# Kernel optimization log

Measured on AMD Instinct MI355X. Metric: run time of the kernel, lower is better.

The kernel has to match this reference:

```python
import jax, jax.numpy as jnp
import numpy as np

N = 50000          # nodes
E = 800000         # edges (avg degree 16)
F_IN = 64          # node feature dim
F_EDGE = 8         # edge feature dim (carried through, unused by EdgeConv)
DIMS = [64, 64, 64, 8]   # hidden layers + final num_classes layer (no BN)
EPS = 1e-5


def mish(x):
    return x * jnp.tanh(jax.nn.softplus(x))


def _init_layer(key, din, dout):
    k1, k2, k3, k4 = jax.random.split(key, 4)
    s1 = 1.0 / np.sqrt(2 * din)
    s2 = 1.0 / np.sqrt(dout)
    w1 = jax.random.uniform(k1, (2 * din, dout), jnp.float32, -s1, s1)
    b1 = jax.random.uniform(k2, (dout,), jnp.float32, -s1, s1)
    w2 = jax.random.uniform(k3, (dout, dout), jnp.float32, -s2, s2)
    b2 = jax.random.uniform(k4, (dout,), jnp.float32, -s2, s2)
    return w1, b1, w2, b2


def setup_inputs() -> dict:
    key = jax.random.key(0)
    ks = jax.random.split(key, 8)
    inp = {
        "x": jax.random.normal(ks[0], (N, F_IN), jnp.float32),
        "edge_index": jax.random.randint(ks[1], (2, E), 0, N, jnp.int32),
        "edge_attr": jax.random.normal(ks[2], (E, F_EDGE), jnp.float32),
    }
    din = F_IN
    for l, dout in enumerate(DIMS):
        w1, b1, w2, b2 = _init_layer(jax.random.fold_in(ks[3], l), din, dout)
        inp[f"w1_{l}"] = w1
        inp[f"b1_{l}"] = b1
        inp[f"w2_{l}"] = w2
        inp[f"b2_{l}"] = b2
        if l < len(DIMS) - 1:  # BN on all but final classifier layer
            inp[f"g_{l}"] = jnp.ones((dout,), jnp.float32)
            inp[f"be_{l}"] = jnp.zeros((dout,), jnp.float32)
        din = dout
    return inp


def _forward(x, edge_index, params):
    src = edge_index[0]
    dst = edge_index[1]
    for (w1, b1, w2, b2, g, be) in params:
        xi = x[dst]                       # [E, din] target feats
        xj = x[src]                       # [E, din] source feats
        m = jnp.concatenate([xi, xj - xi], axis=-1)   # [E, 2*din]
        h = mish(m @ w1 + b1) @ w2 + b2               # [E, dout]
        agg = jax.ops.segment_max(h, dst, num_segments=N)
        x = jnp.where(jnp.isfinite(agg), agg, 0.0)    # empty segments -> 0
        if g is not None:                 # BatchNorm1d, batch stats (train fwd)
            mu = x.mean(axis=0)
            var = x.var(axis=0)
            x = (x - mu) * jax.lax.rsqrt(var + EPS) * g + be
    return x


def reference(x, edge_index, edge_attr,
              w1_0, b1_0, w2_0, b2_0, g_0, be_0,
              w1_1, b1_1, w2_1, b2_1, g_1, be_1,
              w1_2, b1_2, w2_2, b2_2, g_2, be_2,
              w1_3, b1_3, w2_3, b2_3):
    params = [
        (w1_0, b1_0, w2_0, b2_0, g_0, be_0),
        (w1_1, b1_1, w2_1, b2_1, g_1, be_1),
        (w1_2, b1_2, w2_2, b2_2, g_2, be_2),
        (w1_3, b1_3, w2_3, b2_3, None, None),
    ]
    return _forward(x, edge_index, params)
```

## Files before the change

### kernel.cpp

```cpp
#include <hip/hip_runtime.h>
#include <hip/hip_bf16.h>
#include <math.h>

#define NN 50000
#define EE 800000
#define NT (EE / 16)
#define NTN (NN / 16)

#define NBLK64 1536
#define NW64 (NBLK64 * 4)
#define B64 (NT / NW64)
#define R64 (NT % NW64)

#define NBF 196
#define NWF (NBF * 4)

typedef short s8v __attribute__((ext_vector_type(8)));
typedef float f4v __attribute__((ext_vector_type(4)));

__device__ __forceinline__ short f2bf(float f) {
    unsigned u = __float_as_uint(f);
    u += 0x7fffu + ((u >> 16) & 1u);
    return (short)(u >> 16);
}

__device__ __forceinline__ unsigned enc(float f) {
    unsigned u = __float_as_uint(f);
    return (u & 0x80000000u) ? ~u : (u | 0x80000000u);
}
__device__ __forceinline__ float dec(unsigned k) {
    if (k == 0u) return 0.0f;
    unsigned u = (k & 0x80000000u) ? (k & 0x7fffffffu) : ~k;
    return __uint_as_float(u);
}

__device__ __forceinline__ float mish_fast(float v) {
    float t = __expf(v);
    float s = t * (t + 2.0f);
    float r = v * s * __builtin_amdgcn_rcpf(s + 2.0f);
    return (v > 15.0f) ? v : r;
}

#define MFMA16(a, b, c) __builtin_amdgcn_mfma_f32_16x16x32_bf16(a, b, c, 0, 0, 0)


#define NBS 196

__global__ __launch_bounds__(256) void scan_part(const int* __restrict__ cnt,
                                                 int* __restrict__ part) {
    int t = threadIdx.x, i = blockIdx.x * 256 + t;
    __shared__ int ps[256];
    ps[t] = (i < NN) ? cnt[i] : 0;
    __syncthreads();
    for (int off = 128; off > 0; off >>= 1) {
        if (t < off) ps[t] += ps[t + off];
        __syncthreads();
    }
    if (t == 0) part[blockIdx.x] = ps[0];
}

__global__ __launch_bounds__(256) void scan_top(int* __restrict__ part) {
    int t = threadIdx.x;
    int v = (t < NBS) ? part[t] : 0;
    __shared__ int ps[256];
    ps[t] = v;
    __syncthreads();
    for (int off = 1; off < 256; off <<= 1) {
        int u = (t >= off) ? ps[t - off] : 0;
        __syncthreads();
        ps[t] += u;
        __syncthreads();
    }
    if (t < NBS) part[t] = ps[t] - v;
}

__global__ __launch_bounds__(256) void scan_fin(const int* __restrict__ cnt,
                                                const int* __restrict__ part,
                                                int* __restrict__ row_off,
                                                int* __restrict__ cur) {
    int t = threadIdx.x, i = blockIdx.x * 256 + t;
    int v = (i < NN) ? cnt[i] : 0;
    __shared__ int ps[256];
    ps[t] = v;
    __syncthreads();
    for (int off = 1; off < 256; off <<= 1) {
        int u = (t >= off) ? ps[t - off] : 0;
        __syncthreads();
        ps[t] += u;
        __syncthreads();
    }
    int excl = ps[t] - v + part[blockIdx.x];
    if (i < NN) {
        row_off[i] = excl;
        cur[i] = excl;
        if (i == NN - 1) row_off[NN] = excl + v;
    }
}

__global__ __launch_bounds__(256) void scatter_k(const int* __restrict__ ei,
                                                 int* __restrict__ cur,
                                                 int* __restrict__ csr_src,
                                                 int* __restrict__ csr_dst) {
    int e = blockIdx.x * 256 + threadIdx.x;
    if (e < EE) {
        int d = ei[EE + e];
        int p = atomicAdd(&cur[d], 1);
        csr_src[p] = ei[e];
        csr_dst[p] = d;
    }
}


__global__ __launch_bounds__(256)
void cvt_a0(const float* __restrict__ x, const float* __restrict__ w1,
            const float* __restrict__ b1, const int* __restrict__ ei,
            unsigned short* __restrict__ xb, float* __restrict__ a0,
            unsigned* __restrict__ y, unsigned* __restrict__ y8,
            int* __restrict__ cnt) {
    const int tid = threadIdx.x;
    const int lane = tid & 63;
    const int wid = blockIdx.x * 4 + (tid >> 6);
    const int i = lane & 15, q = lane >> 4;
    s8v wf[4][2];
#pragma unroll
    for (int nb = 0; nb < 4; nb++)
#pragma unroll
        for (int kh = 0; kh < 2; kh++)
#pragma unroll
            for (int j = 0; j < 8; j++) {
                int k = kh * 32 + q * 8 + j, n = nb * 16 + i;
                wf[nb][kh][j] = f2bf(w1[k * 64 + n] - w1[(64 + k) * 64 + n]);
            }
    float bia[4];
#pragma unroll
    for (int nb = 0; nb < 4; nb++) bia[nb] = b1[nb * 16 + i];

    for (int t = wid; t < NTN; t += NWF) {
        const int row = t * 16 + i;
        const float* xr = x + (size_t)row * 64 + q * 8;
        f4v x0 = *(const f4v*)xr,        f1 = *(const f4v*)(xr + 4);
        f4v x2 = *(const f4v*)(xr + 32), x3 = *(const f4v*)(xr + 36);
        s8v af0, af1;
#pragma unroll
        for (int j = 0; j < 4; j++) {
            af0[j] = f2bf(x0[j]); af0[4 + j] = f2bf(f1[j]);
            af1[j] = f2bf(x2[j]); af1[4 + j] = f2bf(x3[j]);
        }
        unsigned short* xw = xb + (size_t)row * 64 + q * 8;
        *(s8v*)xw = af0;
        *(s8v*)(xw + 32) = af1;
        const int rowq = t * 16 + q * 4;
#pragma unroll
        for (int nb = 0; nb < 4; nb++) {
            f4v c = {0.f, 0.f, 0.f, 0.f};
            c = MFMA16(af0, wf[nb][0], c);
            c = MFMA16(af1, wf[nb][1], c);
#pragma unroll
            for (int r = 0; r < 4; r++)
                a0[(size_t)(rowq + r) * 64 + i * 4 + nb] = c[r] + bia[nb];
        }
    }
    const int gt = blockIdx.x * 256 + tid, gs = NBF * 256;
    const uint4 z4 = {0u, 0u, 0u, 0u};
    uint4* y4 = (uint4*)y;
    uint4* y84 = (uint4*)y8;
    for (int idx = gt; idx < NN * 16; idx += gs) y4[idx] = z4;
    for (int idx = gt; idx < NN * 2; idx += gs)  y84[idx] = z4;
    for (int e = gt; e < EE; e += gs) atomicAdd(&cnt[ei[EE + e]], 1);
}


__global__ __launch_bounds__(256)
void bn_a0_64(unsigned* __restrict__ yk, const float* __restrict__ st,
              const float* __restrict__ g, const float* __restrict__ be,
              const float* __restrict__ w1n, const float* __restrict__ b1n,
              unsigned short* __restrict__ xbout, float* __restrict__ a0out) {
    __shared__ float sa[64], sb[64];
    const int tid = threadIdx.x;
    if (tid < 64) {
        float mu  = st[tid] * (1.0f / NN);
        float var = st[64 + tid] * (1.0f / NN) - mu * mu;
        float sc  = rsqrtf(var + 1e-5f) * g[tid];
        sa[tid] = sc;
        sb[tid] = be[tid] - mu * sc;
    }
    __syncthreads();
    const int lane = tid & 63;
    const int wid = blockIdx.x * 4 + (tid >> 6);
    const int i = lane & 15, q = lane >> 4;

    s8v wf[4][2];
#pragma unroll
    for (int nb = 0; nb < 4; nb++)
#pragma unroll
        for (int kh = 0; kh < 2; kh++)
#pragma unroll
            for (int j = 0; j < 8; j++) {
                int k = kh * 32 + q * 8 + j, n = nb * 16 + i;
                wf[nb][kh][j] = f2bf(w1n[k * 64 + n] - w1n[(64 + k) * 64 + n]);
            }
    float bia[4];
#pragma unroll
    for (int nb = 0; nb < 4; nb++) bia[nb] = b1n[nb * 16 + i];

    f4v a00 = *(const f4v*)(sa + q * 8),      a01 = *(const f4v*)(sa + q * 8 + 4);
    f4v a10 = *(const f4v*)(sa + 32 + q * 8), a11 = *(const f4v*)(sa + 36 + q * 8);
    f4v b00 = *(const f4v*)(sb + q * 8),      b01 = *(const f4v*)(sb + q * 8 + 4);
    f4v b10 = *(const f4v*)(sb + 32 + q * 8), b11 = *(const f4v*)(sb + 36 + q * 8);

    const uint4 z4 = {0u, 0u, 0u, 0u};
    for (int t = wid; t < NTN; t += NWF) {
        const int row = t * 16 + i;
        unsigned* yr = yk + (size_t)row * 64 + q * 8;
        uint4 u0 = *(const uint4*)yr,        u1 = *(const uint4*)(yr + 4);
        uint4 u2 = *(const uint4*)(yr + 32), u3 = *(const uint4*)(yr + 36);
        s8v af0, af1;
        af0[0] = f2bf(dec(u0.x) * a00[0] + b00[0]);
        af0[1] = f2bf(dec(u0.y) * a00[1] + b00[1]);
        af0[2] = f2bf(dec(u0.z) * a00[2] + b00[2]);
        af0[3] = f2bf(dec(u0.w) * a00[3] + b00[3]);
        af0[4] = f2bf(dec(u1.x) * a01[0] + b01[0]);
        af0[5] = f2bf(dec(u1.y) * a01[1] + b01[1]);
        af0[6] = f2bf(dec(u1.z) * a01[2] + b01[2]);
        af0[7] = f2bf(dec(u1.w) * a01[3] + b01[3]);
        af1[0] = f2bf(dec(u2.x) * a10[0] + b10[0]);
        af1[1] = f2bf(dec(u2.y) * a10[1] + b10[1]);
        af1[2] = f2bf(dec(u2.z) * a10[2] + b10[2]);
        af1[3] = f2bf(dec(u2.w) * a10[3] + b10[3]);
        af1[4] = f2bf(dec(u3.x) * a11[0] + b11[0]);
        af1[5] = f2bf(dec(u3.y) * a11[1] + b11[1]);
        af1[6] = f2bf(dec(u3.z) * a11[2] + b11[2]);
        af1[7] = f2bf(dec(u3.w) * a11[3] + b11[3]);

        unsigned short* xw = xbout + (size_t)row * 64 + q * 8;
        *(s8v*)xw = af0;
        *(s8v*)(xw + 32) = af1;
        *(uint4*)yr = z4;        *(uint4*)(yr + 4) = z4;
        *(uint4*)(yr + 32) = z4; *(uint4*)(yr + 36) = z4;

        const int rowq = t * 16 + q * 4;
#pragma unroll
        for (int nb = 0; nb < 4; nb++) {
            f4v c = {0.f, 0.f, 0.f, 0.f};
            c = MFMA16(af0, wf[nb][0], c);
            c = MFMA16(af1, wf[nb][1], c);
#pragma unroll
            for (int r = 0; r < 4; r++)
                a0out[(size_t)(rowq + r) * 64 + i * 4 + nb] = c[r] + bia[nb];
        }
    }
}


__global__ __launch_bounds__(256)
void bn_a0_8(unsigned* __restrict__ yk, const float* __restrict__ st,
             const float* __restrict__ g, const float* __restrict__ be,
             const float* __restrict__ w1n, const float* __restrict__ b1n,
             unsigned short* __restrict__ xbout, float* __restrict__ a08) {
    __shared__ float sa[64], sb[64];
    const int tid = threadIdx.x;
    if (tid < 64) {
        float mu  = st[tid] * (1.0f / NN);
        float var = st[64 + tid] * (1.0f / NN) - mu * mu;
        float sc  = rsqrtf(var + 1e-5f) * g[tid];
        sa[tid] = sc;
        sb[tid] = be[tid] - mu * sc;
    }
    __syncthreads();
    const int lane = tid & 63;
    const int wid = blockIdx.x * 4 + (tid >> 6);
    const int i = lane & 15, q = lane >> 4;

    s8v wf[2];
#pragma unroll
    for (int kh = 0; kh < 2; kh++)
#pragma unroll
        for (int j = 0; j < 8; j++) {
            int k = kh * 32 + q * 8 + j;
            wf[kh][j] = (i < 8) ? f2bf(w1n[k * 8 + i] - w1n[(64 + k) * 8 + i]) : (short)0;
        }
    const float bia = (i < 8) ? b1n[i] : 0.0f;

    f4v a00 = *(const f4v*)(sa + q * 8),      a01 = *(const f4v*)(sa + q * 8 + 4);
    f4v a10 = *(const f4v*)(sa + 32 + q * 8), a11 = *(const f4v*)(sa + 36 + q * 8);
    f4v b00 = *(const f4v*)(sb + q * 8),      b01 = *(const f4v*)(sb + q * 8 + 4);
    f4v b10 = *(const f4v*)(sb + 32 + q * 8), b11 = *(const f4v*)(sb + 36 + q * 8);

    for (int t = wid; t < NTN; t += NWF) {
        const int row = t * 16 + i;
        const unsigned* yr = yk + (size_t)row * 64 + q * 8;
        uint4 u0 = *(const uint4*)yr,        u1 = *(const uint4*)(yr + 4);
        uint4 u2 = *(const uint4*)(yr + 32), u3 = *(const uint4*)(yr + 36);
        s8v af0, af1;
        af0[0] = f2bf(dec(u0.x) * a00[0] + b00[0]);
        af0[1] = f2bf(dec(u0.y) * a00[1] + b00[1]);
        af0[2] = f2bf(dec(u0.z) * a00[2] + b00[2]);
        af0[3] = f2bf(dec(u0.w) * a00[3] + b00[3]);
        af0[4] = f2bf(dec(u1.x) * a01[0] + b01[0]);
        af0[5] = f2bf(dec(u1.y) * a01[1] + b01[1]);
        af0[6] = f2bf(dec(u1.z) * a01[2] + b01[2]);
        af0[7] = f2bf(dec(u1.w) * a01[3] + b01[3]);
        af1[0] = f2bf(dec(u2.x) * a10[0] + b10[0]);
        af1[1] = f2bf(dec(u2.y) * a10[1] + b10[1]);
        af1[2] = f2bf(dec(u2.z) * a10[2] + b10[2]);
        af1[3] = f2bf(dec(u2.w) * a10[3] + b10[3]);
        af1[4] = f2bf(dec(u3.x) * a11[0] + b11[0]);
        af1[5] = f2bf(dec(u3.y) * a11[1] + b11[1]);
        af1[6] = f2bf(dec(u3.z) * a11[2] + b11[2]);
        af1[7] = f2bf(dec(u3.w) * a11[3] + b11[3]);

        unsigned short* xw = xbout + (size_t)row * 64 + q * 8;
        *(s8v*)xw = af0;
        *(s8v*)(xw + 32) = af1;

        f4v c = {0.f, 0.f, 0.f, 0.f};
        c = MFMA16(af0, wf[0], c);
        c = MFMA16(af1, wf[1], c);
        if (i < 8) {
            const int rowq = t * 16 + q * 4;
#pragma unroll
            for (int r = 0; r < 4; r++)
                a08[(size_t)(rowq + r) * 8 + i] = c[r] + bia;
        }
    }
}


__global__ __launch_bounds__(256)
void edge_mfma64(const unsigned short* __restrict__ xb, const float* __restrict__ a0,
                 const float* __restrict__ w1, const float* __restrict__ w2,
                 const float* __restrict__ b2,
                 const int* __restrict__ csr_src, const int* __restrict__ csr_dst,
                 unsigned* __restrict__ y) {
    __shared__ float uld[4][16 * 68];
    __shared__ int dseg[4][2][20];
    __shared__ short w2l[8 * 64 * 8];
    const int lane = threadIdx.x & 63;
    const int wv = threadIdx.x >> 6;
    const int wid = blockIdx.x * 4 + wv;
    const int i = lane & 15, q = lane >> 4;
    float* up = &uld[wv][0];

    s8v w1f[4][2];
#pragma unroll
    for (int nb = 0; nb < 4; nb++)
#pragma unroll
        for (int kh = 0; kh < 2; kh++)
#pragma unroll
            for (int j = 0; j < 8; j++) {
                int k = kh * 32 + q * 8 + j, n = nb * 16 + i;
                w1f[nb][kh][j] = f2bf(w1[(64 + k) * 64 + n]);
            }
    {
        const int nb = wv;
#pragma unroll
        for (int kh = 0; kh < 2; kh++) {
            s8v uu;
#pragma unroll
            for (int j = 0; j < 8; j++) {
                int k = kh * 32 + q * 8 + j;
                uu[j] = f2bf(w2[k * 64 + nb * 16 + i]);
            }
            *(s8v*)(w2l + ((nb * 2 + kh) * 64 + lane) * 8) = uu;
        }
    }
    __syncthreads();

    const float b2c = b2[lane];

    int t = wid * B64 + (wid < R64 ? wid : R64);
    const int tend = t + B64 + (wid < R64 ? 1 : 0);

    s8v af0_c, af1_c;
    {
        int s0 = csr_src[t * 16 + i];
        const unsigned short* xr = xb + (size_t)s0 * 64;
        af0_c = *(const s8v*)(xr + q * 8);
        af1_c = *(const s8v*)(xr + 32 + q * 8);
    }
    int src_n = (t + 1 < tend) ? csr_src[(t + 1) * 16 + i] : 0;
    if (lane < 17) {
        int e = t * 16 + lane;
        dseg[wv][t & 1][lane] = (e < EE) ? csr_dst[e] : -1;
    }
    asm volatile("s_waitcnt lgkmcnt(0)" ::: "memory");
    int dq_c[4];
#pragma unroll
    for (int r = 0; r < 4; r++) dq_c[r] = dseg[wv][t & 1][q * 4 + r];
    f4v a0r_c[4];
#pragma unroll
    for (int r = 0; r < 4; r++)
        a0r_c[r] = *(const f4v*)(a0 + (size_t)dq_c[r] * 64 + i * 4);

    float run = -INFINITY;

    for (; t < tend; t++) {
        const bool has_n = (t + 1) < tend;
        int* dsg = &dseg[wv][t & 1][0];
        int* dsg_n = &dseg[wv][(t + 1) & 1][0];

        if (has_n && lane < 17) {
            int e = (t + 1) * 16 + lane;
            dsg_n[lane] = (e < EE) ? csr_dst[e] : -1;
        }
        s8v af0_n = {0,0,0,0,0,0,0,0}, af1_n = {0,0,0,0,0,0,0,0};
        if (has_n) {
            const unsigned short* xr = xb + (size_t)src_n * 64;
            af0_n = *(const s8v*)(xr + q * 8);
            af1_n = *(const s8v*)(xr + 32 + q * 8);
        }
        int src_nn = (t + 2 < tend) ? csr_src[(t + 2) * 16 + i] : 0;

        f4v c0 = {0.f, 0.f, 0.f, 0.f}, c1 = c0, c2 = c0, c3 = c0;
        c0 = MFMA16(af0_c, w1f[0][0], c0); c0 = MFMA16(af1_c, w1f[0][1], c0);
        c1 = MFMA16(af0_c, w1f[1][0], c1); c1 = MFMA16(af1_c, w1f[1][1], c1);
        c2 = MFMA16(af0_c, w1f[2][0], c2); c2 = MFMA16(af1_c, w1f[2][1], c2);
        c3 = MFMA16(af0_c, w1f[3][0], c3); c3 = MFMA16(af1_c, w1f[3][1], c3);

        asm volatile("" ::: "memory");
#pragma unroll
        for (int r = 0; r < 4; r++) {
            const int ro = (q * 4 + r) * 68 + i;
            up[ro +  0] = mish_fast(c0[r] + a0r_c[r][0]);
            up[ro + 16] = mish_fast(c1[r] + a0r_c[r][1]);
            up[ro + 32] = mish_fast(c2[r] + a0r_c[r][2]);
            up[ro + 48] = mish_fast(c3[r] + a0r_c[r][3]);
        }
        asm volatile("s_waitcnt lgkmcnt(0)" ::: "memory");

        int dq_n[4];
        f4v a0r_n[4];
        if (has_n) {
#pragma unroll
            for (int r = 0; r < 4; r++) dq_n[r] = dsg_n[q * 4 + r];
#pragma unroll
            for (int r = 0; r < 4; r++)
                a0r_n[r] = *(const f4v*)(a0 + (size_t)dq_n[r] * 64 + i * 4);
        }

        s8v uf[2];
#pragma unroll
        for (int kh = 0; kh < 2; kh++) {
            const f4v* rp = (const f4v*)(up + i * 68 + kh * 32 + q * 8);
            f4v v0 = rp[0], v1 = rp[1];
            s8v uu;
            uu[0] = f2bf(v0[0]); uu[1] = f2bf(v0[1]);
            uu[2] = f2bf(v0[2]); uu[3] = f2bf(v0[3]);
            uu[4] = f2bf(v1[0]); uu[5] = f2bf(v1[1]);
            uu[6] = f2bf(v1[2]); uu[7] = f2bf(v1[3]);
            uf[kh] = uu;
        }
        asm volatile("" ::: "memory");

        f4v cc[4];
#pragma unroll
        for (int nb = 0; nb < 4; nb++) {
            s8v b0 = *(const s8v*)(w2l + ((nb * 2 + 0) * 64 + lane) * 8);
            s8v b1v = *(const s8v*)(w2l + ((nb * 2 + 1) * 64 + lane) * 8);
            f4v c = {0.f, 0.f, 0.f, 0.f};
            c = MFMA16(uf[0], b0, c);
            c = MFMA16(uf[1], b1v, c);
            cc[nb] = c;
        }

#pragma unroll
        for (int nb = 0; nb < 4; nb++)
#pragma unroll
            for (int r = 0; r < 4; r++)
                up[(q * 4 + r) * 68 + nb * 16 + i] = cc[nb][r];
        asm volatile("s_waitcnt lgkmcnt(0)" ::: "memory");

        float v[16];
#pragma unroll
        for (int row = 0; row < 16; row++) v[row] = up[row * 68 + lane];

        int dcur = __builtin_amdgcn_readfirstlane(dsg[0]);
#pragma unroll
        for (int row = 0; row < 16; row++) {
            run = fmaxf(run, v[row]);
            int dn = (row < 15)
                     ? __builtin_amdgcn_readfirstlane(dsg[row + 1])
                     : (has_n ? __builtin_amdgcn_readfirstlane(dsg[16]) : -1);
            if (dcur != dn) {
                atomicMax(&y[(size_t)dcur * 64 + lane], enc(run + b2c));
                run = -INFINITY;
            }
            dcur = dn;
        }
        asm volatile("s_waitcnt lgkmcnt(0)" ::: "memory");

        src_n = src_nn;
        af0_c = af0_n; af1_c = af1_n;
#pragma unroll
        for (int r = 0; r < 4; r++) { dq_c[r] = dq_n[r]; a0r_c[r] = a0r_n[r]; }
    }
}


__global__ __launch_bounds__(256)
void edge_mfma16(const unsigned short* __restrict__ xb, const float* __restrict__ a0,
                 const float* __restrict__ w1, const float* __restrict__ w2,
                 const float* __restrict__ b2,
                 const int* __restrict__ csr_src, const int* __restrict__ csr_dst,
                 unsigned* __restrict__ y8) {
    __shared__ float uld[4][16 * 20];
    __shared__ int dseg[4][2][20];
    const int lane = threadIdx.x & 63;
    const int wv = threadIdx.x >> 6;
    const int wid = blockIdx.x * 4 + wv;
    const int i = lane & 15, q = lane >> 4;
    float* up = &uld[wv][0];

    s8v w1f[2], w2f;
#pragma unroll
    for (int kh = 0; kh < 2; kh++)
#pragma unroll
        for (int j = 0; j < 8; j++) {
            int k = kh * 32 + q * 8 + j;
            w1f[kh][j] = (i < 8) ? f2bf(w1[(64 + k) * 8 + i]) : (short)0;
        }
#pragma unroll
    for (int j = 0; j < 8; j++)
        w2f[j] = (q == 0 && i < 8) ? f2bf(w2[j * 8 + i]) : (short)0;
    const float b2c = (lane < 8) ? b2[lane] : 0.0f;

    int t = wid * B64 + (wid < R64 ? wid : R64);
    const int tend = t + B64 + (wid < R64 ? 1 : 0);

    s8v af0_c, af1_c;
    {
        int s0 = csr_src[t * 16 + i];
        const unsigned short* xr = xb + (size_t)s0 * 64;
        af0_c = *(const s8v*)(xr + q * 8);
        af1_c = *(const s8v*)(xr + 32 + q * 8);
    }
    int src_n = (t + 1 < tend) ? csr_src[(t + 1) * 16 + i] : 0;
    if (lane < 17) {
        int e = t * 16 + lane;
        dseg[wv][t & 1][lane] = (e < EE) ? csr_dst[e] : -1;
    }
    asm volatile("s_waitcnt lgkmcnt(0)" ::: "memory");
    int dq_c[4];
#pragma unroll
    for (int r = 0; r < 4; r++) dq_c[r] = dseg[wv][t & 1][q * 4 + r];
    float av_c[4];
#pragma unroll
    for (int r = 0; r < 4; r++)
        av_c[r] = (i < 8) ? a0[(size_t)dq_c[r] * 8 + i] : 0.0f;

    float run = -INFINITY;

    for (; t < tend; t++) {
        const bool has_n = (t + 1) < tend;
        int* dsg = &dseg[wv][t & 1][0];
        int* dsg_n = &dseg[wv][(t + 1) & 1][0];

        if (has_n && lane < 17) {
            int e = (t + 1) * 16 + lane;
            dsg_n[lane] = (e < EE) ? csr_dst[e] : -1;
        }
        s8v af0_n = {0,0,0,0,0,0,0,0}, af1_n = {0,0,0,0,0,0,0,0};
        if (has_n) {
            const unsigned short* xr = xb + (size_t)src_n * 64;
            af0_n = *(const s8v*)(xr + q * 8);
            af1_n = *(const s8v*)(xr + 32 + q * 8);
        }
        int src_nn = (t + 2 < tend) ? csr_src[(t + 2) * 16 + i] : 0;

        f4v c = {0.f, 0.f, 0.f, 0.f};
        c = MFMA16(af0_c, w1f[0], c);
        c = MFMA16(af1_c, w1f[1], c);

        asm volatile("" ::: "memory");
#pragma unroll
        for (int r = 0; r < 4; r++)
            up[(q * 4 + r) * 20 + i] = mish_fast(c[r] + av_c[r]);
        asm volatile("s_waitcnt lgkmcnt(0)" ::: "memory");

        int dq_n[4];
        float av_n[4] = {0, 0, 0, 0};
        if (has_n) {
#pragma unroll
            for (int r = 0; r < 4; r++) dq_n[r] = dsg_n[q * 4 + r];
#pragma unroll
            for (int r = 0; r < 4; r++)
                av_n[r] = (i < 8) ? a0[(size_t)dq_n[r] * 8 + i] : 0.0f;
        }

        s8v uf = {0,0,0,0,0,0,0,0};
        if (q < 2) {
            const f4v* rp = (const f4v*)(up + i * 20 + q * 8);
            f4v v0 = rp[0], v1 = rp[1];
            uf[0] = f2bf(v0[0]); uf[1] = f2bf(v0[1]);
            uf[2] = f2bf(v0[2]); uf[3] = f2bf(v0[3]);
            uf[4] = f2bf(v1[0]); uf[5] = f2bf(v1[1]);
            uf[6] = f2bf(v1[2]); uf[7] = f2bf(v1[3]);
        }
        asm volatile("" ::: "memory");

        f4v cc = {0.f, 0.f, 0.f, 0.f};
        cc = MFMA16(uf, w2f, cc);

#pragma unroll
        for (int r = 0; r < 4; r++)
            up[(q * 4 + r) * 20 + i] = cc[r];
        asm volatile("s_waitcnt lgkmcnt(0)" ::: "memory");

        float v[16];
#pragma unroll
        for (int row = 0; row < 16; row++) v[row] = up[row * 20 + (lane & 7)];

        int dcur = dsg[0];
#pragma unroll
        for (int row = 0; row < 16; row++) {
            run = fmaxf(run, v[row]);
            int dn = (row < 15) ? dsg[row + 1] : (has_n ? dsg[16] : -1);
            if (dcur != dn) {
                if (lane < 8)
                    atomicMax(&y8[(size_t)dcur * 8 + lane], enc(run + b2c));
                run = -INFINITY;
            }
            dcur = dn;
        }
        asm volatile("s_waitcnt lgkmcnt(0)" ::: "memory");

        src_n = src_nn;
        af0_c = af0_n; af1_c = af1_n;
#pragma unroll
        for (int r = 0; r < 4; r++) av_c[r] = av_n[r];
    }
}


__global__ __launch_bounds__(256)
void bn_stats(const unsigned* __restrict__ yk, float* __restrict__ st) {
    const int tid = threadIdx.x;
    const int c4 = (tid & 15) * 4;
    const int grp = tid >> 4;
    float s0 = 0, s1 = 0, s2 = 0, s3 = 0;
    float q0 = 0, q1 = 0, q2 = 0, q3 = 0;
    for (int n = blockIdx.x * 16 + grp; n < NN; n += gridDim.x * 16) {
        uint4 u = *(const uint4*)(yk + (size_t)n * 64 + c4);
        float v0 = dec(u.x), v1 = dec(u.y), v2 = dec(u.z), v3 = dec(u.w);
        s0 += v0; s1 += v1; s2 += v2; s3 += v3;
        q0 = fmaf(v0, v0, q0); q1 = fmaf(v1, v1, q1);
        q2 = fmaf(v2, v2, q2); q3 = fmaf(v3, v3, q3);
    }
    __shared__ float ls[256][4], lq[256][4];
    ls[tid][0] = s0; ls[tid][1] = s1; ls[tid][2] = s2; ls[tid][3] = s3;
    lq[tid][0] = q0; lq[tid][1] = q1; lq[tid][2] = q2; lq[tid][3] = q3;
    __syncthreads();
    if (tid < 64) {
        const int cg = tid >> 2, ce = tid & 3;
        float ss = 0, qq = 0;
        for (int g = 0; g < 16; g++) {
            ss += ls[g * 16 + cg][ce];
            qq += lq[g * 16 + cg][ce];
        }
        atomicAdd(&st[cg * 4 + ce], ss);
        atomicAdd(&st[64 + cg * 4 + ce], qq);
    }
}

__global__ __launch_bounds__(256)
void decode_out(const unsigned* __restrict__ y8, float* __restrict__ out) {
    int idx = blockIdx.x * 256 + threadIdx.x;
    if (idx < NN * 8) out[idx] = dec(y8[idx]);
}


extern "C" void kernel_launch(void* const* d_in, const int* in_sizes, int n_in,
                              void* d_out, int out_size, void* d_ws, size_t ws_size,
                              hipStream_t stream) {
    const float* x0 = (const float*)d_in[0];
    const int*   ei = (const int*)d_in[1];
    const float* w1[4] = {(const float*)d_in[3],  (const float*)d_in[9],
                          (const float*)d_in[15], (const float*)d_in[21]};
    const float* b1[4] = {(const float*)d_in[4],  (const float*)d_in[10],
                          (const float*)d_in[16], (const float*)d_in[22]};
    const float* w2[4] = {(const float*)d_in[5],  (const float*)d_in[11],
                          (const float*)d_in[17], (const float*)d_in[23]};
    const float* b2[4] = {(const float*)d_in[6],  (const float*)d_in[12],
                          (const float*)d_in[18], (const float*)d_in[24]};
    const float* gg[3] = {(const float*)d_in[7],  (const float*)d_in[13],
                          (const float*)d_in[19]};
    const float* be[3] = {(const float*)d_in[8],  (const float*)d_in[14],
                          (const float*)d_in[20]};

    char* p = (char*)d_ws;
    auto alloc = [&](size_t bytes) -> char* {
        char* r = p;
        p += (bytes + 255) & ~(size_t)255;
        return r;
    };
    int*      cnt     = (int*)alloc((size_t)NN * 4);
    int*      part    = (int*)alloc((size_t)NBS * 4);
    int*      row_off = (int*)alloc((size_t)(NN + 1) * 4);
    int*      cur     = (int*)alloc((size_t)NN * 4);
    int*      csr_s   = (int*)alloc((size_t)EE * 4);
    int*      csr_d   = (int*)alloc((size_t)EE * 4);
    float*    st      = (float*)alloc(3 * 128 * 4);
    float*    a0      = (float*)alloc((size_t)NN * 64 * 4);
    unsigned* y       = (unsigned*)alloc((size_t)NN * 64 * 4);
    unsigned* y8      = (unsigned*)alloc((size_t)NN * 8 * 4);
    unsigned short* xb0 = (unsigned short*)alloc((size_t)NN * 64 * 2);
    unsigned short* xbA = (unsigned short*)alloc((size_t)NN * 64 * 2);
    unsigned short* xbB = xb0;

    hipMemsetAsync(cnt, 0, (size_t)NN * 4, stream);
    hipMemsetAsync(st, 0, 3 * 128 * 4, stream);

    cvt_a0<<<NBF, 256, 0, stream>>>(x0, w1[0], b1[0], ei, xb0, a0, y, y8, cnt);

    scan_part<<<NBS, 256, 0, stream>>>(cnt, part);
    scan_top<<<1, 256, 0, stream>>>(part);
    scan_fin<<<NBS, 256, 0, stream>>>(cnt, part, row_off, cur);
    scatter_k<<<(EE + 255) / 256, 256, 0, stream>>>(ei, cur, csr_s, csr_d);

    edge_mfma64<<<NBLK64, 256, 0, stream>>>(xb0, a0, w1[0], w2[0], b2[0],
                                            csr_s, csr_d, y);
    bn_stats<<<256, 256, 0, stream>>>(y, st);
    bn_a0_64<<<NBF, 256, 0, stream>>>(y, st, gg[0], be[0], w1[1], b1[1], xbA, a0);

    edge_mfma64<<<NBLK64, 256, 0, stream>>>(xbA, a0, w1[1], w2[1], b2[1],
                                            csr_s, csr_d, y);
    bn_stats<<<256, 256, 0, stream>>>(y, st + 128);
    bn_a0_64<<<NBF, 256, 0, stream>>>(y, st + 128, gg[1], be[1], w1[2], b1[2], xbB, a0);

    edge_mfma64<<<NBLK64, 256, 0, stream>>>(xbB, a0, w1[2], w2[2], b2[2],
                                            csr_s, csr_d, y);
    bn_stats<<<256, 256, 0, stream>>>(y, st + 256);
    bn_a0_8<<<NBF, 256, 0, stream>>>(y, st + 256, gg[2], be[2], w1[3], b1[3], xbA, a0);

    edge_mfma16<<<NBLK64, 256, 0, stream>>>(xbA, a0, w1[3], w2[3], b2[3],
                                            csr_s, csr_d, y8);
    decode_out<<<(NN * 8 + 255) / 256, 256, 0, stream>>>(y8, (float*)d_out);
}
```

Before: 512.7 us.

## Pre-reduce segment max in MFMA registers before LDS transpose in edge_mfma64

Replaces the per-tile LDS write of all 16x64 edge outputs and the sequential 16-row scan with a two-level reduction. Each lane first folds its 4 accumulator rows by destination, using wave-wide any-checks and atomics on segment breaks. Only the 4 partial maxima per column are then staged through LDS and scanned, carrying the running max across tiles with a final flush atomic. This cuts LDS traffic and scalar readfirstlane work. The cost is divergent atomics inside the register scan and reliance on lanes within a quad sharing each row's destination indices.

```diff
diff --git a/kernel.cpp b/kernel.cpp
--- a/kernel.cpp
+++ b/kernel.cpp
@@ -340,6 +340,7 @@
     const int wid = blockIdx.x * 4 + wv;
     const int i = lane & 15, q = lane >> 4;
     float* up = &uld[wv][0];
+    float* spw = up;
 
     s8v w1f[4][2];
 #pragma unroll
@@ -366,7 +367,9 @@
     }
     __syncthreads();
 
-    const float b2c = b2[lane];
+    const float b2s = b2[lane];
+    const float b2n0 = b2[i],      b2n1 = b2[16 + i];
+    const float b2n2 = b2[32 + i], b2n3 = b2[48 + i];
 
     int t = wid * B64 + (wid < R64 ? wid : R64);
     const int tend = t + B64 + (wid < R64 ? 1 : 0);
@@ -379,10 +382,7 @@
         af1_c = *(const s8v*)(xr + 32 + q * 8);
     }
     int src_n = (t + 1 < tend) ? csr_src[(t + 1) * 16 + i] : 0;
-    if (lane < 17) {
-        int e = t * 16 + lane;
-        dseg[wv][t & 1][lane] = (e < EE) ? csr_dst[e] : -1;
-    }
+    if (lane < 16) dseg[wv][t & 1][lane] = csr_dst[t * 16 + lane];
     asm volatile("s_waitcnt lgkmcnt(0)" ::: "memory");
     int dq_c[4];
 #pragma unroll
@@ -392,17 +392,16 @@
     for (int r = 0; r < 4; r++)
         a0r_c[r] = *(const f4v*)(a0 + (size_t)dq_c[r] * 64 + i * 4);
 
-    float run = -INFINITY;
+    float runC = -INFINITY;
+    int dcC = dseg[wv][t & 1][0];
 
     for (; t < tend; t++) {
         const bool has_n = (t + 1) < tend;
-        int* dsg = &dseg[wv][t & 1][0];
+        const int* dsg = &dseg[wv][t & 1][0];
         int* dsg_n = &dseg[wv][(t + 1) & 1][0];
 
-        if (has_n && lane < 17) {
-            int e = (t + 1) * 16 + lane;
-            dsg_n[lane] = (e < EE) ? csr_dst[e] : -1;
-        }
+        if (has_n && lane < 16) dsg_n[lane] = csr_dst[(t + 1) * 16 + lane];
+
         s8v af0_n = {0,0,0,0,0,0,0,0}, af1_n = {0,0,0,0,0,0,0,0};
         if (has_n) {
             const unsigned short* xr = xb + (size_t)src_n * 64;
@@ -463,30 +462,59 @@
             cc[nb] = c;
         }
 
-#pragma unroll
-        for (int nb = 0; nb < 4; nb++)
-#pragma unroll
-            for (int r = 0; r < 4; r++)
-                up[(q * 4 + r) * 68 + nb * 16 + i] = cc[nb][r];
+        float r0 = cc[0][0], r1 = cc[1][0], r2 = cc[2][0], r3 = cc[3][0];
+
+#define SCAN_STEP(RR)                                                        \
+        {                                                                    \
+            bool mm = (dq_c[RR] != dq_c[RR - 1]);                            \
+            if (__any(mm)) {                                                 \
+                if (mm) {                                                    \
+                    size_t bse = (size_t)dq_c[RR - 1] * 64 + i;              \
+                    atomicMax(&y[bse],      enc(r0 + b2n0));                 \
+                    atomicMax(&y[bse + 16], enc(r1 + b2n1));                 \
+                    atomicMax(&y[bse + 32], enc(r2 + b2n2));                 \
+                    atomicMax(&y[bse + 48], enc(r3 + b2n3));                 \
+                }                                                            \
+                r0 = mm ? cc[0][RR] : fmaxf(r0, cc[0][RR]);                  \
+                r1 = mm ? cc[1][RR] : fmaxf(r1, cc[1][RR]);                  \
+                r2 = mm ? cc[2][RR] : fmaxf(r2, cc[2][RR]);                  \
+                r3 = mm ? cc[3][RR] : fmaxf(r3, cc[3][RR]);                  \
+            } else {                                                         \
+                r0 = fmaxf(r0, cc[0][RR]); r1 = fmaxf(r1, cc[1][RR]);        \
+                r2 = fmaxf(r2, cc[2][RR]); r3 = fmaxf(r3, cc[3][RR]);        \
+            }                                                                \
+        }
+        SCAN_STEP(1)
+        SCAN_STEP(2)
+        SCAN_STEP(3)
+#undef SCAN_STEP
+
+        spw[q * 68 +       i] = r0;
+        spw[q * 68 + 16 +  i] = r1;
+        spw[q * 68 + 32 +  i] = r2;
+        spw[q * 68 + 48 +  i] = r3;
         asm volatile("s_waitcnt lgkmcnt(0)" ::: "memory");
 
-        float v[16];
-#pragma unroll
-        for (int row = 0; row < 16; row++) v[row] = up[row * 68 + lane];
-
-        int dcur = __builtin_amdgcn_readfirstlane(dsg[0]);
-#pragma unroll
-        for (int row = 0; row < 16; row++) {
-            run = fmaxf(run, v[row]);
-            int dn = (row < 15)
-                     ? __builtin_amdgcn_readfirstlane(dsg[row + 1])
-                     : (has_n ? __builtin_amdgcn_readfirstlane(dsg[16]) : -1);
-            if (dcur != dn) {
-                atomicMax(&y[(size_t)dcur * 64 + lane], enc(run + b2c));
-                run = -INFINITY;
-            }
-            dcur = dn;
-        }
+        float v0 = spw[lane],        v1 = spw[68 + lane];
+        float v2s = spw[136 + lane], v3s = spw[204 + lane];
+        int e0 = dsg[3], e1 = dsg[7], e2 = dsg[11], e3 = dsg[15];
+
+        if (e0 != dcC) {
+            atomicMax(&y[(size_t)dcC * 64 + lane], enc(runC + b2s));
+            runC = v0; dcC = e0;
+        } else runC = fmaxf(runC, v0);
+        if (e1 != dcC) {
+            atomicMax(&y[(size_t)dcC * 64 + lane], enc(runC + b2s));
+            runC = v1; dcC = e1;
+        } else runC = fmaxf(runC, v1);
+        if (e2 != dcC) {
+            atomicMax(&y[(size_t)dcC * 64 + lane], enc(runC + b2s));
+            runC = v2s; dcC = e2;
+        } else runC = fmaxf(runC, v2s);
+        if (e3 != dcC) {
+            atomicMax(&y[(size_t)dcC * 64 + lane], enc(runC + b2s));
+            runC = v3s; dcC = e3;
+        } else runC = fmaxf(runC, v3s);
         asm volatile("s_waitcnt lgkmcnt(0)" ::: "memory");
 
         src_n = src_nn;
@@ -494,6 +522,7 @@
 #pragma unroll
         for (int r = 0; r < 4; r++) { dq_c[r] = dq_n[r]; a0r_c[r] = a0r_n[r]; }
     }
+    atomicMax(&y[(size_t)dcC * 64 + lane], enc(runC + b2s));
 }
 
 
```

Result: faster. 499.1 us (-2.7%).
